# Optimization experiments

Measured on AMD Instinct MI355X. Metric: run time of the kernel, lower is better.

## Reference

```python
import math
import jax, jax.numpy as jnp
import numpy as np

SHAPES = ((100, 150), (50, 75), (25, 38), (13, 19))  # (H, W) per level
N_HEADS = 8
N_POINTS = 4
EMBED = 256


def setup_inputs() -> dict:
    key = jax.random.key(0)
    ks = jax.random.split(key, 8)
    bs = 2
    L = len(SHAPES)
    nv = sum(h * w for h, w in SHAPES)  # 19947
    nq = nv
    d = EMBED
    query = jax.random.normal(ks[0], (bs, nq, d), jnp.float32)
    value = jax.random.normal(ks[1], (bs, nv, d), jnp.float32)
    reference_points = jax.random.uniform(ks[2], (bs, nq, L, 2), dtype=jnp.float32)
    spatial_shapes = jnp.asarray(np.array(SHAPES, np.int32))
    # sampling_offsets bias: directional grid init, as in the module's init_weights
    thetas = np.arange(N_HEADS, dtype=np.float64) * (2.0 * math.pi / N_HEADS)
    grid = np.stack([np.cos(thetas), np.sin(thetas)], -1)
    grid = grid / np.abs(grid).max(-1, keepdims=True)
    grid = np.tile(grid[:, None, None, :], (1, L, N_POINTS, 1))
    grid = grid * np.arange(1, N_POINTS + 1, dtype=np.float64)[None, None, :, None]
    b_off = jnp.asarray(grid.reshape(-1), jnp.float32)  # (h*L*p*2,)
    # small random weights (zero-init in module would make offsets constant)
    W_off = 0.01 * jax.random.normal(ks[3], (N_HEADS * L * N_POINTS * 2, d), jnp.float32)
    W_attn = 0.01 * jax.random.normal(ks[4], (N_HEADS * L * N_POINTS, d), jnp.float32)
    b_attn = jnp.zeros((N_HEADS * L * N_POINTS,), jnp.float32)
    s = 1.0 / math.sqrt(d)
    W_val = s * jax.random.normal(ks[5], (d, d), jnp.float32)
    b_val = jnp.zeros((d,), jnp.float32)
    W_out = s * jax.random.normal(ks[6], (d, d), jnp.float32)
    b_out = jnp.zeros((d,), jnp.float32)
    return dict(query=query, value=value, reference_points=reference_points,
                spatial_shapes=spatial_shapes, W_off=W_off, b_off=b_off,
                W_attn=W_attn, b_attn=b_attn, W_val=W_val, b_val=b_val,
                W_out=W_out, b_out=b_out)


def _msda(value, shapes, loc, attn):
    """Multi-scale deformable attention core.
    value: (bs, nv, h, hd)  loc: (bs, nq, h, L, p, 2) in [0,1]
    attn:  (bs, nq, h, L, p) -> returns (bs, nq, h*hd)
    Equivalent to grid_sample(bilinear, padding='zeros', align_corners=False).
    """
    bs, nq, h, L, p, _ = loc.shape
    hd = value.shape[-1]
    out = jnp.zeros((bs, nq, h, hd), value.dtype)
    start = 0
    for lvl in range(L):
        H, W = int(shapes[lvl, 0]), int(shapes[lvl, 1])
        v = value[:, start:start + H * W]               # (bs, H*W, h, hd)
        l = loc[:, :, :, lvl]                           # (bs, nq, h, p, 2)
        # align_corners=False unnormalization: x = loc*W - 0.5
        x = l[..., 0] * W - 0.5
        y = l[..., 1] * H - 0.5
        x0 = jnp.floor(x)
        y0 = jnp.floor(y)
        wx = x - x0
        wy = y - y0
        x0i = x0.astype(jnp.int32)
        y0i = y0.astype(jnp.int32)

        def corner(xi, yi, w):
            valid = (xi >= 0) & (xi < W) & (yi >= 0) & (yi < H)
            idx = jnp.clip(yi, 0, H - 1) * W + jnp.clip(xi, 0, W - 1)  # (bs,nq,h,p)
            idxf = idx.transpose(0, 1, 3, 2).reshape(bs, nq * p, h)
            g = jnp.take_along_axis(v, idxf[..., None], axis=1)        # (bs,nq*p,h,hd)
            g = g.reshape(bs, nq, p, h, hd).transpose(0, 1, 3, 2, 4)   # (bs,nq,h,p,hd)
            return g * jnp.where(valid, w, 0.0)[..., None]

        samp = (corner(x0i, y0i, (1 - wx) * (1 - wy))
                + corner(x0i + 1, y0i, wx * (1 - wy))
                + corner(x0i, y0i + 1, (1 - wx) * wy)
                + corner(x0i + 1, y0i + 1, wx * wy))
        out = out + (samp * attn[:, :, :, lvl, :, None]).sum(3)
        start += H * W
    return out.reshape(bs, nq, h * hd)


def reference(query, value, reference_points, spatial_shapes,
              W_off, b_off, W_attn, b_attn, W_val, b_val, W_out, b_out):
    shapes = np.asarray(spatial_shapes)  # static level shapes
    bs, nq, d = query.shape
    L = shapes.shape[0]
    h, p = N_HEADS, N_POINTS
    hd = d // h
    off = (query @ W_off.T + b_off).reshape(bs, nq, h, L, p, 2)
    aw = (query @ W_attn.T + b_attn).reshape(bs, nq, h, L * p)
    aw = jax.nn.softmax(aw, axis=-1).reshape(bs, nq, h, L, p)
    v = (value @ W_val.T + b_val).reshape(bs, -1, h, hd)
    # offset normalizer is (W, H) per level
    norm = jnp.asarray(np.stack([shapes[:, 1], shapes[:, 0]], -1), query.dtype)  # (L,2)
    loc = reference_points[:, :, None, :, None, :] + off / norm[None, None, None, :, None, :]
    out = _msda(v, shapes, loc, aw)          # (bs, nq, d)
    return out @ W_out.T + b_out
```

## Files before the change

### kernel.cpp

```cpp
#include <hip/hip_runtime.h>
#include <hip/hip_bf16.h>
#include <hip/hip_fp16.h>
#include <cmath>


typedef __attribute__((ext_vector_type(8))) short short8;
typedef __attribute__((ext_vector_type(4))) float f32x4;

#define MREAL 39894
#define MP    39936
#define NQ2   39894

__device__ __forceinline__ unsigned short f2bf(float f) {
    union { float f; unsigned u; } x; x.f = f;
    unsigned r = (x.u + 0x7fffu + ((x.u >> 16) & 1u)) >> 16;
    return (unsigned short)r;
}
__device__ __forceinline__ unsigned cvt_pk_bf16(float lo, float hi) {
    unsigned r;
    asm("v_cvt_pk_bf16_f32 %0, %1, %2" : "=v"(r) : "v"(lo), "v"(hi));
    return r;
}

template<int AMODE, int OUTMODE>
__device__ __forceinline__ void gemm_body(
    short* __restrict__ As, short* __restrict__ Bs,
    const void* __restrict__ A, const float* __restrict__ B1,
    const float* __restrict__ B2, int nsplit,
    const float* __restrict__ bias, const float* __restrict__ bias2, int bsplit,
    void* __restrict__ Cout, int ldc, int m_t, int n_t, int Mstore)
{
    const int tid = threadIdx.x;
    const int m0 = m_t * 128;
    const int n0 = n_t * 128;
    const int w  = tid >> 6;
    const int l  = tid & 63;
    const int wm = w >> 2, wn = w & 3;
    const int lr = l & 15;
    const int lk = (l >> 4) * 8;

    const int srow = tid >> 2;
    const int skc  = (tid & 3) * 8;
    const int bkc  = (tid & 3) * 32;

    const int gn = n0 + srow;
    const float* Bp = (gn < nsplit) ? B1 + (size_t)gn * 256
                                    : B2 + (size_t)(gn - nsplit) * 256;

    f32x4 acc[4][2] = {};

    float4 pa0, pa1;
    short8 pab;

    auto loadA = [&](int ks) {
        if constexpr (AMODE == 1) {
            const float* Af = (const float*)A;
            const int r = min(m0 + srow, MREAL - 1);
            const float* p = Af + (size_t)r * 256 + ks * 32 + skc;
            pa0 = *reinterpret_cast<const float4*>(p);
            pa1 = *reinterpret_cast<const float4*>(p + 4);
        } else {
            const short* Ab = (const short*)A;
            pab = *reinterpret_cast<const short8*>(Ab + (size_t)(m0 + srow) * 256 + ks * 32 + skc);
        }
    };
    auto writeA = [&]() {
        if constexpr (AMODE == 1) {
            uint4 q;
            q.x = cvt_pk_bf16(pa0.x, pa0.y); q.y = cvt_pk_bf16(pa0.z, pa0.w);
            q.z = cvt_pk_bf16(pa1.x, pa1.y); q.w = cvt_pk_bf16(pa1.z, pa1.w);
            *reinterpret_cast<uint4*>(&As[srow * 40 + skc]) = q;
        } else {
            *reinterpret_cast<short8*>(&As[srow * 40 + skc]) = pab;
        }
    };
    auto loadB = [&](int half) {
        const float* p = Bp + half * 128 + bkc;
#pragma unroll
        for (int i = 0; i < 4; ++i) {
            float4 x = *reinterpret_cast<const float4*>(p + i * 8);
            float4 y = *reinterpret_cast<const float4*>(p + i * 8 + 4);
            uint4 q;
            q.x = cvt_pk_bf16(x.x, x.y); q.y = cvt_pk_bf16(x.z, x.w);
            q.z = cvt_pk_bf16(y.x, y.y); q.w = cvt_pk_bf16(y.z, y.w);
            *reinterpret_cast<uint4*>(&Bs[srow * 136 + bkc + i * 8]) = q;
        }
    };

    loadB(0);
    loadA(0);
    writeA();
    loadA(1);
    __syncthreads();

#pragma unroll
    for (int ks = 0; ks < 8; ++ks) {
        const int kk = (ks & 3) * 32;
        short8 bfr0 = *reinterpret_cast<const short8*>(&Bs[(wn * 32 + lr) * 136 + kk + lk]);
        short8 bfr1 = *reinterpret_cast<const short8*>(&Bs[(wn * 32 + 16 + lr) * 136 + kk + lk]);
#pragma unroll
        for (int mi = 0; mi < 4; ++mi) {
            short8 afr = *reinterpret_cast<const short8*>(&As[(wm * 64 + mi * 16 + lr) * 40 + lk]);
            acc[mi][0] = __builtin_amdgcn_mfma_f32_16x16x32_bf16(afr, bfr0, acc[mi][0], 0, 0, 0);
            acc[mi][1] = __builtin_amdgcn_mfma_f32_16x16x32_bf16(afr, bfr1, acc[mi][1], 0, 0, 0);
        }
        if (ks < 7) {
            __syncthreads();
            writeA();
            if (ks == 3) loadB(1);
            if (ks < 6) loadA(ks + 2);
            __syncthreads();
        }
    }

    const int r4 = (l >> 4) * 4;
#pragma unroll
    for (int ni = 0; ni < 2; ++ni) {
        const int col = n0 + wn * 32 + ni * 16 + lr;
        const float bv = (col < bsplit) ? bias[col] : bias2[col - bsplit];
#pragma unroll
        for (int mi = 0; mi < 4; ++mi) {
#pragma unroll
            for (int r = 0; r < 4; ++r) {
                const int row = m0 + wm * 64 + mi * 16 + r4 + r;
                if (row < Mstore) {
                    const float val = acc[mi][ni][r] + bv;
                    if constexpr (OUTMODE == 2) {
                        union { __half h; unsigned short u; } cv; cv.h = __float2half(val);
                        reinterpret_cast<unsigned short*>(Cout)[(size_t)row * ldc + col] = cv.u;
                    } else if constexpr (OUTMODE == 3) {
                        union { __half h; unsigned short u; } cv; cv.h = __float2half(val);
                        reinterpret_cast<unsigned short*>(Cout)[(size_t)(col >> 5) * MP * 32
                                                               + (size_t)row * 32 + (col & 31)] = cv.u;
                    } else {
                        reinterpret_cast<float*>(Cout)[(size_t)row * ldc + col] = val;
                    }
                }
            }
        }
    }
}

__global__ __launch_bounds__(512) void gemm_fused(
    const float* __restrict__ value, const float* __restrict__ query,
    const float* __restrict__ woff, const float* __restrict__ wattn,
    const float* __restrict__ wval,
    const float* __restrict__ b_off, const float* __restrict__ b_attn,
    const float* __restrict__ b_val,
    short* __restrict__ vplanes, short* __restrict__ oabuf)
{
    __shared__ short As[128 * 40];
    __shared__ short Bs[128 * 136];

    const int bid = blockIdx.x;
    if (bid < 624) {
        const int m_t = ((bid >> 4) << 3) | (bid & 7);
        const int n_t = (bid >> 3) & 1;
        gemm_body<1, 3>(As, Bs, value, wval, wval, 256,
                        b_val, b_val, 1 << 30, vplanes, 256, m_t, n_t, MP);
    } else {
        const int b = bid - 624;
        const int m_t = ((b / 24) << 3) | (b & 7);
        const int n_t = (b >> 3) % 3;
        gemm_body<1, 2>(As, Bs, query, woff, wattn, 256,
                        b_off, b_attn, 256, oabuf, 384, m_t, n_t, MP);
    }
}

__global__ __launch_bounds__(512) void gemm_out(
    const short* __restrict__ sbuf, const float* __restrict__ wout,
    const float* __restrict__ b_out, float* __restrict__ out)
{
    __shared__ short As[128 * 40];
    __shared__ short Bs[128 * 136];
    const int bid = blockIdx.x;
    const int m_t = ((bid >> 4) << 3) | (bid & 7);
    const int n_t = (bid >> 3) & 1;
    gemm_body<0, 0>(As, Bs, sbuf, wout, wout, 256,
                    b_out, b_out, 1 << 30, out, 256, m_t, n_t, MREAL);
}

__global__ __launch_bounds__(256) void msda_sample7(
    const char* __restrict__ vplanes,
    const __half* __restrict__ offattn,
    const float* __restrict__ ref,
    uint4* __restrict__ sampled)
{
    __shared__ __attribute__((aligned(16))) unsigned s_w[16][68];
    __shared__ __attribute__((aligned(16))) int      s_idx[16][68];
    __shared__ float s_inv[16];

    const int bid = blockIdx.x;
    const int h = bid & 7;
    const int qbase = (bid >> 3) * 16;
    const int tid = threadIdx.x;
    const int qp = tid >> 4;

    {
        const int s = tid & 15;
        const int lvl = s >> 2;
        const int qi = qbase + qp;
        const bool live = (qi < NQ2);

        const int Hs[4] = {100, 50, 25, 13};
        const int Ws[4] = {150, 75, 38, 19};
        const int st[4] = {0, 15000, 18750, 19700};

        float e = 1.f;
        unsigned wv[4] = {0, 0, 0, 0};
        int      iv[4] = {0, 0, 0, 0};
        if (live) {
            const __half* oa = offattn + (size_t)qi * 384;
            unsigned short lu = __builtin_nontemporal_load(
                reinterpret_cast<const unsigned short*>(oa + 256 + h * 16 + s));
            union { unsigned short u; __half h; } lh; lh.u = lu;
            e = __expf(__half2float(lh.h));
            unsigned ou = __builtin_nontemporal_load(
                reinterpret_cast<const unsigned*>(oa + h * 32 + 2 * s));
            union { unsigned u; __half2 h2; } oh; oh.u = ou;
            const float ox = __low2float(oh.h2), oy = __high2float(oh.h2);
            const float2 r2 = *reinterpret_cast<const float2*>(ref + (size_t)qi * 8 + lvl * 2);

            const int H = Hs[lvl], W = Ws[lvl];
            const float x = r2.x * (float)W + ox - 0.5f;
            const float y = r2.y * (float)H + oy - 0.5f;
            const float x0f = floorf(x), y0f = floorf(y);
            const float wx = x - x0f, wy = y - y0f;
            const int x0 = (int)x0f, y0 = (int)y0f;
            const int base = ((qi >= 19947) ? 19947 : 0) + st[lvl];

            const float w00 = (1.f - wx) * (1.f - wy), w01 = wx * (1.f - wy);
            const float w10 = (1.f - wx) * wy,         w11 = wx * wy;
            const bool vx0 = (x0 >= 0) & (x0 < W), vx1 = (x0 + 1 >= 0) & (x0 + 1 < W);
            const bool vy0 = (y0 >= 0) & (y0 < H), vy1 = (y0 + 1 >= 0) & (y0 + 1 < H);
            const int xc0 = min(max(x0, 0), W - 1), xc1 = min(max(x0 + 1, 0), W - 1);
            const int yc0 = min(max(y0, 0), H - 1), yc1 = min(max(y0 + 1, 0), H - 1);
            iv[0] = (base + yc0 * W + xc0) << 6;
            iv[1] = (base + yc0 * W + xc1) << 6;
            iv[2] = (base + yc1 * W + xc0) << 6;
            iv[3] = (base + yc1 * W + xc1) << 6;
            union { __half2 h; unsigned u; } cw;
            cw.h = __float2half2_rn((vx0 & vy0) ? e * w00 : 0.f); wv[0] = cw.u;
            cw.h = __float2half2_rn((vx1 & vy0) ? e * w01 : 0.f); wv[1] = cw.u;
            cw.h = __float2half2_rn((vx0 & vy1) ? e * w10 : 0.f); wv[2] = cw.u;
            cw.h = __float2half2_rn((vx1 & vy1) ? e * w11 : 0.f); wv[3] = cw.u;
        }
        float den = e;
        den += __shfl_xor(den, 1, 64);
        den += __shfl_xor(den, 2, 64);
        den += __shfl_xor(den, 4, 64);
        den += __shfl_xor(den, 8, 64);
        if (s == 0) s_inv[qp] = 1.f / den;
#pragma unroll
        for (int c = 0; c < 4; ++c) {
            s_w[qp][c * 16 + s] = wv[c];
            s_idx[qp][c * 16 + s] = iv[c];
        }
    }
    __syncthreads();

    const int l = tid & 63;
    const int c4 = (l >> 2) & 3;
    const int cp4 = l & 3;
    const int qi = qbase + qp;

    const char* vb = vplanes + (size_t)h * (MP * 64) + cp4 * 16;

    const unsigned* wp = &s_w[qp][c4 * 16];
    const int*      ip = &s_idx[qp][c4 * 16];

    const int4 ia = *reinterpret_cast<const int4*>(ip + 0);
    const int4 ib = *reinterpret_cast<const int4*>(ip + 4);
    const int4 ic = *reinterpret_cast<const int4*>(ip + 8);
    const int4 id = *reinterpret_cast<const int4*>(ip + 12);
    const uint4 wa = *reinterpret_cast<const uint4*>(wp + 0);
    const uint4 wb = *reinterpret_cast<const uint4*>(wp + 4);
    const uint4 wc = *reinterpret_cast<const uint4*>(wp + 8);
    const uint4 wd = *reinterpret_cast<const uint4*>(wp + 12);

    const uint4 p0  = *reinterpret_cast<const uint4*>(vb + ia.x);
    const uint4 p1  = *reinterpret_cast<const uint4*>(vb + ia.y);
    const uint4 p2  = *reinterpret_cast<const uint4*>(vb + ia.z);
    const uint4 p3  = *reinterpret_cast<const uint4*>(vb + ia.w);
    const uint4 p4  = *reinterpret_cast<const uint4*>(vb + ib.x);
    const uint4 p5  = *reinterpret_cast<const uint4*>(vb + ib.y);
    const uint4 p6  = *reinterpret_cast<const uint4*>(vb + ib.z);
    const uint4 p7  = *reinterpret_cast<const uint4*>(vb + ib.w);
    const uint4 p8  = *reinterpret_cast<const uint4*>(vb + ic.x);
    const uint4 p9  = *reinterpret_cast<const uint4*>(vb + ic.y);
    const uint4 p10 = *reinterpret_cast<const uint4*>(vb + ic.z);
    const uint4 p11 = *reinterpret_cast<const uint4*>(vb + ic.w);
    const uint4 p12 = *reinterpret_cast<const uint4*>(vb + id.x);
    const uint4 p13 = *reinterpret_cast<const uint4*>(vb + id.y);
    const uint4 p14 = *reinterpret_cast<const uint4*>(vb + id.z);
    const uint4 p15 = *reinterpret_cast<const uint4*>(vb + id.w);

    union HU { __half2 h; unsigned u; };
    __half2 acc[4];
#pragma unroll
    for (int i = 0; i < 4; ++i) acc[i] = __float2half2_rn(0.f);

#define FMA4(P, WU) { HU va, ww; ww.u = (WU); \
    va.u = (P).x; acc[0] = __hfma2(va.h, ww.h, acc[0]); \
    va.u = (P).y; acc[1] = __hfma2(va.h, ww.h, acc[1]); \
    va.u = (P).z; acc[2] = __hfma2(va.h, ww.h, acc[2]); \
    va.u = (P).w; acc[3] = __hfma2(va.h, ww.h, acc[3]); }

    FMA4(p0,  wa.x) FMA4(p1,  wa.y) FMA4(p2,  wa.z) FMA4(p3,  wa.w)
    FMA4(p4,  wb.x) FMA4(p5,  wb.y) FMA4(p6,  wb.z) FMA4(p7,  wb.w)
    FMA4(p8,  wc.x) FMA4(p9,  wc.y) FMA4(p10, wc.z) FMA4(p11, wc.w)
    FMA4(p12, wd.x) FMA4(p13, wd.y) FMA4(p14, wd.z) FMA4(p15, wd.w)
#undef FMA4

#pragma unroll
    for (int i = 0; i < 4; ++i) {
        HU a; a.h = acc[i];
        HU b;
        b.u = __shfl_xor(a.u, 4, 64); a.h = __hadd2(a.h, b.h);
        b.u = __shfl_xor(a.u, 8, 64); a.h = __hadd2(a.h, b.h);
        acc[i] = a.h;
    }

    if (c4 == 0 && qi < NQ2) {
        const float inv = s_inv[qp];
        uint4 o;
        o.x = ((unsigned)f2bf(__high2float(acc[0]) * inv) << 16) | (unsigned)f2bf(__low2float(acc[0]) * inv);
        o.y = ((unsigned)f2bf(__high2float(acc[1]) * inv) << 16) | (unsigned)f2bf(__low2float(acc[1]) * inv);
        o.z = ((unsigned)f2bf(__high2float(acc[2]) * inv) << 16) | (unsigned)f2bf(__low2float(acc[2]) * inv);
        o.w = ((unsigned)f2bf(__high2float(acc[3]) * inv) << 16) | (unsigned)f2bf(__low2float(acc[3]) * inv);
        sampled[(size_t)qi * 32 + h * 4 + cp4] = o;
    }
}

extern "C" void kernel_launch(void* const* d_in, const int* in_sizes, int n_in,
                              void* d_out, int out_size, void* d_ws, size_t ws_size,
                              hipStream_t stream) {
    const float* query  = (const float*)d_in[0];
    const float* value  = (const float*)d_in[1];
    const float* refp   = (const float*)d_in[2];
    const float* W_off  = (const float*)d_in[4];
    const float* b_off  = (const float*)d_in[5];
    const float* W_attn = (const float*)d_in[6];
    const float* b_attn = (const float*)d_in[7];
    const float* W_val  = (const float*)d_in[8];
    const float* b_val  = (const float*)d_in[9];
    const float* W_out  = (const float*)d_in[10];
    const float* b_out  = (const float*)d_in[11];
    float* out = (float*)d_out;

    short* vplanes = (short*)d_ws;
    short* oabuf   = vplanes + (size_t)MP * 256;
    short* sbuf    = oabuf + (size_t)MP * 384;

    gemm_fused<<<dim3(624 + 936), dim3(512), 0, stream>>>(
        value, query, W_off, W_attn, W_val, b_off, b_attn, b_val, vplanes, oabuf);

    const int ngroups = (MREAL + 15) / 16;
    msda_sample7<<<dim3(ngroups * 8), dim3(256), 0, stream>>>(
        (const char*)vplanes, (const __half*)oabuf, refp, (uint4*)sbuf);

    gemm_out<<<dim3(624), dim3(512), 0, stream>>>(sbuf, W_out, b_out, out);
}
```

Measured before the change: 147.0 us.

## Double-buffer A tile in GEMMs with deeper prefetch; simplify sampler indexing

The GEMM body now keeps four A chunks in flight in registers and alternates between two LDS A buffers. This removes one of the two barriers per k-step and hides global load latency better. The sampler drops its per-query live branch by clamping the query index, and it switches to unsigned 32-bit offsets from a per-head base, which should let the compiler use cheaper buffer addressing. The cost is more LDS and more registers in the GEMM, which may lower occupancy.

```diff
diff --git a/kernel.cpp b/kernel.cpp
--- a/kernel.cpp
+++ b/kernel.cpp
@@ -24,7 +24,8 @@
 
 template<int AMODE, int OUTMODE>
 __device__ __forceinline__ void gemm_body(
-    short* __restrict__ As, short* __restrict__ Bs,
+    short* __restrict__ As,
+    short* __restrict__ Bs,
     const void* __restrict__ A, const float* __restrict__ B1,
     const float* __restrict__ B2, int nsplit,
     const float* __restrict__ bias, const float* __restrict__ bias2, int bsplit,
@@ -47,31 +48,37 @@
     const float* Bp = (gn < nsplit) ? B1 + (size_t)gn * 256
                                     : B2 + (size_t)(gn - nsplit) * 256;
 
+    const float* Af = nullptr; const short* Ab = nullptr;
+    if constexpr (AMODE == 1) {
+        Af = (const float*)A + (size_t)min(m0 + srow, MREAL - 1) * 256 + skc;
+    } else {
+        Ab = (const short*)A + (size_t)(m0 + srow) * 256 + skc;
+    }
+
     f32x4 acc[4][2] = {};
 
-    float4 pa0, pa1;
-    short8 pab;
-
-    auto loadA = [&](int ks) {
+    float4 ra[4], rb[4];
+    short8 rs[4];
+
+    auto loadSlot = [&](int chunk) {
+        const int s = chunk & 3;
         if constexpr (AMODE == 1) {
-            const float* Af = (const float*)A;
-            const int r = min(m0 + srow, MREAL - 1);
-            const float* p = Af + (size_t)r * 256 + ks * 32 + skc;
-            pa0 = *reinterpret_cast<const float4*>(p);
-            pa1 = *reinterpret_cast<const float4*>(p + 4);
+            ra[s] = *reinterpret_cast<const float4*>(Af + chunk * 32);
+            rb[s] = *reinterpret_cast<const float4*>(Af + chunk * 32 + 4);
         } else {
-            const short* Ab = (const short*)A;
-            pab = *reinterpret_cast<const short8*>(Ab + (size_t)(m0 + srow) * 256 + ks * 32 + skc);
+            rs[s] = *reinterpret_cast<const short8*>(Ab + chunk * 32);
         }
     };
-    auto writeA = [&]() {
+    auto writeSlot = [&](int chunk) {
+        const int s = chunk & 3;
+        short* dst = As + (chunk & 1) * (128 * 40) + srow * 40 + skc;
         if constexpr (AMODE == 1) {
             uint4 q;
-            q.x = cvt_pk_bf16(pa0.x, pa0.y); q.y = cvt_pk_bf16(pa0.z, pa0.w);
-            q.z = cvt_pk_bf16(pa1.x, pa1.y); q.w = cvt_pk_bf16(pa1.z, pa1.w);
-            *reinterpret_cast<uint4*>(&As[srow * 40 + skc]) = q;
+            q.x = cvt_pk_bf16(ra[s].x, ra[s].y); q.y = cvt_pk_bf16(ra[s].z, ra[s].w);
+            q.z = cvt_pk_bf16(rb[s].x, rb[s].y); q.w = cvt_pk_bf16(rb[s].z, rb[s].w);
+            *reinterpret_cast<uint4*>(dst) = q;
         } else {
-            *reinterpret_cast<short8*>(&As[srow * 40 + skc]) = pab;
+            *reinterpret_cast<short8*>(dst) = rs[s];
         }
     };
     auto loadB = [&](int half) {
@@ -88,27 +95,31 @@
     };
 
     loadB(0);
-    loadA(0);
-    writeA();
-    loadA(1);
+    loadSlot(0); loadSlot(1); loadSlot(2); loadSlot(3);
+    writeSlot(0);
     __syncthreads();
 
 #pragma unroll
     for (int ks = 0; ks < 8; ++ks) {
         const int kk = (ks & 3) * 32;
+        const short* Ar = As + (ks & 1) * (128 * 40);
         short8 bfr0 = *reinterpret_cast<const short8*>(&Bs[(wn * 32 + lr) * 136 + kk + lk]);
         short8 bfr1 = *reinterpret_cast<const short8*>(&Bs[(wn * 32 + 16 + lr) * 136 + kk + lk]);
 #pragma unroll
         for (int mi = 0; mi < 4; ++mi) {
-            short8 afr = *reinterpret_cast<const short8*>(&As[(wm * 64 + mi * 16 + lr) * 40 + lk]);
+            short8 afr = *reinterpret_cast<const short8*>(&Ar[(wm * 64 + mi * 16 + lr) * 40 + lk]);
             acc[mi][0] = __builtin_amdgcn_mfma_f32_16x16x32_bf16(afr, bfr0, acc[mi][0], 0, 0, 0);
             acc[mi][1] = __builtin_amdgcn_mfma_f32_16x16x32_bf16(afr, bfr1, acc[mi][1], 0, 0, 0);
         }
-        if (ks < 7) {
+        if (ks == 3) {
+            writeSlot(4);
             __syncthreads();
-            writeA();
-            if (ks == 3) loadB(1);
-            if (ks < 6) loadA(ks + 2);
+            loadB(1);
+            loadSlot(7);
+            __syncthreads();
+        } else if (ks < 7) {
+            writeSlot(ks + 1);
+            if (ks < 3) loadSlot(ks + 4);
             __syncthreads();
         }
     }
@@ -149,7 +160,7 @@
     const float* __restrict__ b_val,
     short* __restrict__ vplanes, short* __restrict__ oabuf)
 {
-    __shared__ short As[128 * 40];
+    __shared__ short As[2 * 128 * 40];
     __shared__ short Bs[128 * 136];
 
     const int bid = blockIdx.x;
@@ -171,7 +182,7 @@
     const short* __restrict__ sbuf, const float* __restrict__ wout,
     const float* __restrict__ b_out, float* __restrict__ out)
 {
-    __shared__ short As[128 * 40];
+    __shared__ short As[2 * 128 * 40];
     __shared__ short Bs[128 * 136];
     const int bid = blockIdx.x;
     const int m_t = ((bid >> 4) << 3) | (bid & 7);
@@ -180,7 +191,7 @@
                     b_out, b_out, 1 << 30, out, 256, m_t, n_t, MREAL);
 }
 
-__global__ __launch_bounds__(256) void msda_sample7(
+__global__ __launch_bounds__(256) void msda_sample8(
     const char* __restrict__ vplanes,
     const __half* __restrict__ offattn,
     const float* __restrict__ ref,
@@ -199,52 +210,49 @@
     {
         const int s = tid & 15;
         const int lvl = s >> 2;
-        const int qi = qbase + qp;
-        const bool live = (qi < NQ2);
+        const int qc = min(qbase + qp, NQ2 - 1);
 
         const int Hs[4] = {100, 50, 25, 13};
         const int Ws[4] = {150, 75, 38, 19};
         const int st[4] = {0, 15000, 18750, 19700};
 
-        float e = 1.f;
-        unsigned wv[4] = {0, 0, 0, 0};
-        int      iv[4] = {0, 0, 0, 0};
-        if (live) {
-            const __half* oa = offattn + (size_t)qi * 384;
-            unsigned short lu = __builtin_nontemporal_load(
-                reinterpret_cast<const unsigned short*>(oa + 256 + h * 16 + s));
-            union { unsigned short u; __half h; } lh; lh.u = lu;
-            e = __expf(__half2float(lh.h));
-            unsigned ou = __builtin_nontemporal_load(
-                reinterpret_cast<const unsigned*>(oa + h * 32 + 2 * s));
-            union { unsigned u; __half2 h2; } oh; oh.u = ou;
-            const float ox = __low2float(oh.h2), oy = __high2float(oh.h2);
-            const float2 r2 = *reinterpret_cast<const float2*>(ref + (size_t)qi * 8 + lvl * 2);
-
-            const int H = Hs[lvl], W = Ws[lvl];
-            const float x = r2.x * (float)W + ox - 0.5f;
-            const float y = r2.y * (float)H + oy - 0.5f;
-            const float x0f = floorf(x), y0f = floorf(y);
-            const float wx = x - x0f, wy = y - y0f;
-            const int x0 = (int)x0f, y0 = (int)y0f;
-            const int base = ((qi >= 19947) ? 19947 : 0) + st[lvl];
-
-            const float w00 = (1.f - wx) * (1.f - wy), w01 = wx * (1.f - wy);
-            const float w10 = (1.f - wx) * wy,         w11 = wx * wy;
-            const bool vx0 = (x0 >= 0) & (x0 < W), vx1 = (x0 + 1 >= 0) & (x0 + 1 < W);
-            const bool vy0 = (y0 >= 0) & (y0 < H), vy1 = (y0 + 1 >= 0) & (y0 + 1 < H);
-            const int xc0 = min(max(x0, 0), W - 1), xc1 = min(max(x0 + 1, 0), W - 1);
-            const int yc0 = min(max(y0, 0), H - 1), yc1 = min(max(y0 + 1, 0), H - 1);
-            iv[0] = (base + yc0 * W + xc0) << 6;
-            iv[1] = (base + yc0 * W + xc1) << 6;
-            iv[2] = (base + yc1 * W + xc0) << 6;
-            iv[3] = (base + yc1 * W + xc1) << 6;
-            union { __half2 h; unsigned u; } cw;
-            cw.h = __float2half2_rn((vx0 & vy0) ? e * w00 : 0.f); wv[0] = cw.u;
-            cw.h = __float2half2_rn((vx1 & vy0) ? e * w01 : 0.f); wv[1] = cw.u;
-            cw.h = __float2half2_rn((vx0 & vy1) ? e * w10 : 0.f); wv[2] = cw.u;
-            cw.h = __float2half2_rn((vx1 & vy1) ? e * w11 : 0.f); wv[3] = cw.u;
-        }
+        const __half* oa = offattn + (size_t)qc * 384;
+        unsigned short lu = __builtin_nontemporal_load(
+            reinterpret_cast<const unsigned short*>(oa + 256 + h * 16 + s));
+        union { unsigned short u; __half h; } lh; lh.u = lu;
+        const float e = __expf(__half2float(lh.h));
+        unsigned ou = __builtin_nontemporal_load(
+            reinterpret_cast<const unsigned*>(oa + h * 32 + 2 * s));
+        union { unsigned u; __half2 h2; } oh; oh.u = ou;
+        const float ox = __low2float(oh.h2), oy = __high2float(oh.h2);
+        const float2 r2 = *reinterpret_cast<const float2*>(ref + (size_t)qc * 8 + lvl * 2);
+
+        const int H = Hs[lvl], W = Ws[lvl];
+        const float x = r2.x * (float)W + ox - 0.5f;
+        const float y = r2.y * (float)H + oy - 0.5f;
+        const float x0f = floorf(x), y0f = floorf(y);
+        const float wx = x - x0f, wy = y - y0f;
+        const int x0 = (int)x0f, y0 = (int)y0f;
+        const int base = ((qc >= 19947) ? 19947 : 0) + st[lvl];
+
+        const float w00 = (1.f - wx) * (1.f - wy), w01 = wx * (1.f - wy);
+        const float w10 = (1.f - wx) * wy,         w11 = wx * wy;
+        const bool vx0 = (x0 >= 0) & (x0 < W), vx1 = (x0 + 1 >= 0) & (x0 + 1 < W);
+        const bool vy0 = (y0 >= 0) & (y0 < H), vy1 = (y0 + 1 >= 0) & (y0 + 1 < H);
+        const int xc0 = min(max(x0, 0), W - 1), xc1 = min(max(x0 + 1, 0), W - 1);
+        const int yc0 = min(max(y0, 0), H - 1), yc1 = min(max(y0 + 1, 0), H - 1);
+        int iv[4];
+        iv[0] = (base + yc0 * W + xc0) << 6;
+        iv[1] = (base + yc0 * W + xc1) << 6;
+        iv[2] = (base + yc1 * W + xc0) << 6;
+        iv[3] = (base + yc1 * W + xc1) << 6;
+        unsigned wv[4];
+        union { __half2 h; unsigned u; } cw;
+        cw.h = __float2half2_rn((vx0 & vy0) ? e * w00 : 0.f); wv[0] = cw.u;
+        cw.h = __float2half2_rn((vx1 & vy0) ? e * w01 : 0.f); wv[1] = cw.u;
+        cw.h = __float2half2_rn((vx0 & vy1) ? e * w10 : 0.f); wv[2] = cw.u;
+        cw.h = __float2half2_rn((vx1 & vy1) ? e * w11 : 0.f); wv[3] = cw.u;
+
         float den = e;
         den += __shfl_xor(den, 1, 64);
         den += __shfl_xor(den, 2, 64);
@@ -262,9 +270,10 @@
     const int l = tid & 63;
     const int c4 = (l >> 2) & 3;
     const int cp4 = l & 3;
+    const int cp8 = cp4 * 16;
     const int qi = qbase + qp;
 
-    const char* vb = vplanes + (size_t)h * (MP * 64) + cp4 * 16;
+    const char* vbase = vplanes + (size_t)h * (MP * 64);
 
     const unsigned* wp = &s_w[qp][c4 * 16];
     const int*      ip = &s_idx[qp][c4 * 16];
@@ -278,22 +287,22 @@
     const uint4 wc = *reinterpret_cast<const uint4*>(wp + 8);
     const uint4 wd = *reinterpret_cast<const uint4*>(wp + 12);
 
-    const uint4 p0  = *reinterpret_cast<const uint4*>(vb + ia.x);
-    const uint4 p1  = *reinterpret_cast<const uint4*>(vb + ia.y);
-    const uint4 p2  = *reinterpret_cast<const uint4*>(vb + ia.z);
-    const uint4 p3  = *reinterpret_cast<const uint4*>(vb + ia.w);
-    const uint4 p4  = *reinterpret_cast<const uint4*>(vb + ib.x);
-    const uint4 p5  = *reinterpret_cast<const uint4*>(vb + ib.y);
-    const uint4 p6  = *reinterpret_cast<const uint4*>(vb + ib.z);
-    const uint4 p7  = *reinterpret_cast<const uint4*>(vb + ib.w);
-    const uint4 p8  = *reinterpret_cast<const uint4*>(vb + ic.x);
-    const uint4 p9  = *reinterpret_cast<const uint4*>(vb + ic.y);
-    const uint4 p10 = *reinterpret_cast<const uint4*>(vb + ic.z);
-    const uint4 p11 = *reinterpret_cast<const uint4*>(vb + ic.w);
-    const uint4 p12 = *reinterpret_cast<const uint4*>(vb + id.x);
-    const uint4 p13 = *reinterpret_cast<const uint4*>(vb + id.y);
-    const uint4 p14 = *reinterpret_cast<const uint4*>(vb + id.z);
-    const uint4 p15 = *reinterpret_cast<const uint4*>(vb + id.w);
+    const uint4 p0  = *reinterpret_cast<const uint4*>(vbase + (unsigned)(ia.x + cp8));
+    const uint4 p1  = *reinterpret_cast<const uint4*>(vbase + (unsigned)(ia.y + cp8));
+    const uint4 p2  = *reinterpret_cast<const uint4*>(vbase + (unsigned)(ia.z + cp8));
+    const uint4 p3  = *reinterpret_cast<const uint4*>(vbase + (unsigned)(ia.w + cp8));
+    const uint4 p4  = *reinterpret_cast<const uint4*>(vbase + (unsigned)(ib.x + cp8));
+    const uint4 p5  = *reinterpret_cast<const uint4*>(vbase + (unsigned)(ib.y + cp8));
+    const uint4 p6  = *reinterpret_cast<const uint4*>(vbase + (unsigned)(ib.z + cp8));
+    const uint4 p7  = *reinterpret_cast<const uint4*>(vbase + (unsigned)(ib.w + cp8));
+    const uint4 p8  = *reinterpret_cast<const uint4*>(vbase + (unsigned)(ic.x + cp8));
+    const uint4 p9  = *reinterpret_cast<const uint4*>(vbase + (unsigned)(ic.y + cp8));
+    const uint4 p10 = *reinterpret_cast<const uint4*>(vbase + (unsigned)(ic.z + cp8));
+    const uint4 p11 = *reinterpret_cast<const uint4*>(vbase + (unsigned)(ic.w + cp8));
+    const uint4 p12 = *reinterpret_cast<const uint4*>(vbase + (unsigned)(id.x + cp8));
+    const uint4 p13 = *reinterpret_cast<const uint4*>(vbase + (unsigned)(id.y + cp8));
+    const uint4 p14 = *reinterpret_cast<const uint4*>(vbase + (unsigned)(id.z + cp8));
+    const uint4 p15 = *reinterpret_cast<const uint4*>(vbase + (unsigned)(id.w + cp8));
 
     union HU { __half2 h; unsigned u; };
     __half2 acc[4];
@@ -356,7 +365,7 @@
         value, query, W_off, W_attn, W_val, b_off, b_attn, b_val, vplanes, oabuf);
 
     const int ngroups = (MREAL + 15) / 16;
-    msda_sample7<<<dim3(ngroups * 8), dim3(256), 0, stream>>>(
+    msda_sample8<<<dim3(ngroups * 8), dim3(256), 0, stream>>>(
         (const char*)vplanes, (const __half*)oabuf, refp, (uint4*)sbuf);
 
     gemm_out<<<dim3(624), dim3(512), 0, stream>>>(sbuf, W_out, b_out, out);
```

Result: faster. 142.4 us (-3.1%).
